# Kernel optimization log

Hardware: AMD Instinct MI355X
Metric: run time of the kernel (lower is better)

## Reference

```python
import jax, jax.numpy as jnp
import numpy as np
from jax import lax

GROUPS = 32
GN_EPS = 1e-3  # keras GroupNormalization default


def setup_inputs() -> dict:
    key = jax.random.key(0)
    ks = jax.random.split(key, 3)
    b, h, w, c = 16, 64, 64, 1024
    cg = c // GROUPS
    x = jax.random.normal(ks[0], (b, h, w, c), dtype=jnp.float32)
    w1 = jax.random.normal(ks[1], (cg, cg), dtype=jnp.float32) * (1.0 / np.sqrt(cg))
    b1 = jnp.zeros((cg,), jnp.float32)
    w3 = jax.random.normal(ks[2], (3, 3, cg, cg), dtype=jnp.float32) * (1.0 / np.sqrt(9 * cg))
    b3 = jnp.zeros((cg,), jnp.float32)
    gn_gamma = jnp.ones((cg,), jnp.float32)
    gn_beta = jnp.zeros((cg,), jnp.float32)
    return {"x": x, "w1": w1, "b1": b1, "w3": w3, "b3": b3,
            "gn_gamma": gn_gamma, "gn_beta": gn_beta}


def reference(x, w1, b1, w3, b3, gn_gamma, gn_beta):
    b, h, w, c = x.shape
    cg = c // GROUPS
    bg = b * GROUPS
    gx = x.reshape(bg, h, w, cg)

    # adaptive pools to 1 along one spatial axis
    x_h = jnp.mean(gx, axis=2, keepdims=True)                      # (bg, h, 1, cg)
    x_w = jnp.transpose(jnp.mean(gx, axis=1, keepdims=True), (0, 2, 1, 3))  # (bg, w, 1, cg)

    # 1x1 conv on concatenated strip (width==1) == matmul over channels
    hw = jnp.concatenate([x_h, x_w], axis=1)                       # (bg, h+w, 1, cg)
    hw = jnp.einsum('bsoc,cd->bsod', hw, w1) + b1
    x_h, x_w = hw[:, :h], hw[:, h:]
    x_w = jnp.transpose(x_w, (0, 2, 1, 3))                         # (bg, 1, w, cg)

    gated = gx * jax.nn.sigmoid(x_h) * jax.nn.sigmoid(x_w)

    # GroupNorm with groups == cg over cg channels -> per-channel norm over (h, w)
    mu = jnp.mean(gated, axis=(1, 2), keepdims=True)
    var = jnp.var(gated, axis=(1, 2), keepdims=True)
    x1 = (gated - mu) * lax.rsqrt(var + GN_EPS) * gn_gamma + gn_beta

    # 3x3 same conv
    x2 = lax.conv_general_dilated(gx, w3, (1, 1), 'SAME',
                                  dimension_numbers=('NHWC', 'HWIO', 'NHWC')) + b3

    # channel attention: softmax over global-avg-pooled channels
    x11 = jax.nn.softmax(jnp.mean(x1, axis=(1, 2)), axis=-1)       # (bg, cg)
    x21 = jax.nn.softmax(jnp.mean(x2, axis=(1, 2)), axis=-1)       # (bg, cg)
    # raw reshape (memory reinterpretation, matches TF code exactly)
    x12 = x2.reshape(bg, cg, h * w)
    x22 = x1.reshape(bg, cg, h * w)

    weights = (jnp.einsum('bc,bcl->bl', x11, x12) +
               jnp.einsum('bc,bcl->bl', x21, x22)).reshape(bg, h, w, 1)
    return (gx * jax.nn.sigmoid(weights)).reshape(b, h, w, c)
```

## Files before the change

### kernel.cpp

```cpp
#include <hip/hip_runtime.h>

typedef __bf16 bf16x8 __attribute__((ext_vector_type(8)));
typedef float floatx4 __attribute__((ext_vector_type(4)));

__device__ __forceinline__ float sigmoidf_(float v) {
    return 1.0f / (1.0f + __expf(-v));
}

extern "C" __global__ __launch_bounds__(512, 4)
void ema_fused(const float* __restrict__ x, const float* __restrict__ w1,
               const float* __restrict__ b1, const float* __restrict__ w3,
               const float* __restrict__ b3, const float* __restrict__ gamma,
               const float* __restrict__ beta, float* __restrict__ out)
{
    __shared__ float sm[17952];
    const int t = threadIdx.x;
    const int b = blockIdx.x;
    const float* gx = x + (size_t)b * 131072;
    float* gout = out + (size_t)b * 131072;

    const int c = t & 31;
    const int k = t >> 5;
    const int lane = t & 63;
    const int wave = t >> 6;
    const int nf = wave & 1;
    const int wbase = (wave >> 1) * 16;
    const int m_ = lane & 15;
    const int q_ = lane >> 4;

    float* rowsum = sm;
    float* colsum = sm + 2112;
    float* G      = sm;
    float* T1     = sm + 4096;
    float* astage = sm + 4224;
    float* shl    = sm + 8192;
    float* swl    = sm + 10240;
    __bf16* ringbase = (__bf16*)(sm + 12288);
    float*  sgbuf    = sm + 12288;
    __bf16* zrow     = (__bf16*)(sm + 16512);
    float* x21    = sm + 17568;
    float* x11    = sm + 17600;
    float* a1v    = sm + 17632;
    float* a0v    = sm + 17664;
    float* b3c    = sm + 17696;
    float* corners= sm + 17728;
    float* Stot   = sm + 17856;
    float* meanx2 = sm + 17888;

    float colacc[4];
#pragma unroll
    for (int i = 0; i < 4; ++i) colacc[i] = 0.f;

    for (int h8 = 0; h8 < 8; ++h8) {
#pragma unroll
        for (int j = 0; j < 8; ++j) {
            int h = h8 * 8 + j;
            float part = 0.f;
#pragma unroll
            for (int i = 0; i < 4; ++i) {
                int w = k + 16 * i;
                float v = gx[(h * 64 + w) * 32 + c];
                colacc[i] += v;
                part += v;
                if ((h == 0 || h == 63) && w == 0)
                    corners[((h == 63) ? 2 : 0) * 32 + c] = v;
                if ((h == 0 || h == 63) && w == 63)
                    corners[((h == 63) ? 3 : 1) * 32 + c] = v;
            }
            astage[(j * 16 + k) * 32 + c] = part;
        }
        __syncthreads();
        if (t < 256) {
            int j2 = t >> 5, c2 = t & 31;
            float s = 0.f;
#pragma unroll
            for (int k2 = 0; k2 < 16; ++k2) s += astage[(j2 * 16 + k2) * 32 + c2];
            rowsum[(h8 * 8 + j2) * 33 + c2] = s;
        }
        __syncthreads();
    }
#pragma unroll
    for (int i = 0; i < 4; ++i) colsum[(k + 16 * i) * 33 + c] = colacc[i];
    __syncthreads();

    {
        const int hh = t >> 3;
        const int d0 = (t & 7) * 4;
        float acch[4], accw[4];
#pragma unroll
        for (int kk = 0; kk < 4; ++kk) { acch[kk] = b1[d0 + kk]; accw[kk] = b1[d0 + kk]; }
        for (int ci = 0; ci < 32; ++ci) {
            float rs = rowsum[hh * 33 + ci] * (1.f / 64.f);
            float cs = colsum[hh * 33 + ci] * (1.f / 64.f);
#pragma unroll
            for (int kk = 0; kk < 4; ++kk) {
                float wv = w1[ci * 32 + d0 + kk];
                acch[kk] += rs * wv;
                accw[kk] += cs * wv;
            }
        }
#pragma unroll
        for (int kk = 0; kk < 4; ++kk) {
            shl[hh * 32 + d0 + kk] = sigmoidf_(acch[kk]);
            swl[hh * 32 + d0 + kk] = sigmoidf_(accw[kk]);
        }
    }
    if (t < 32) {
        float s = 0.f;
        for (int h = 0; h < 64; ++h) s += rowsum[h * 33 + t];
        Stot[t] = s;
        b3c[t] = b3[t];
    }
    __syncthreads();
    if (t < 32) {
        int co = t;
        float acc = 0.f;
        for (int dh = -1; dh <= 1; ++dh)
            for (int dw = -1; dw <= 1; ++dw) {
                int ks = (dh + 1) * 3 + (dw + 1);
                for (int ci = 0; ci < 32; ++ci) {
                    float S = Stot[ci];
                    if (dh == -1) S -= rowsum[63 * 33 + ci];
                    if (dh ==  1) S -= rowsum[ci];
                    if (dw == -1) S -= colsum[63 * 33 + ci];
                    if (dw ==  1) S -= colsum[ci];
                    if (dh == -1 && dw == -1) S += corners[3 * 32 + ci];
                    if (dh == -1 && dw ==  1) S += corners[2 * 32 + ci];
                    if (dh ==  1 && dw == -1) S += corners[1 * 32 + ci];
                    if (dh ==  1 && dw ==  1) S += corners[0 * 32 + ci];
                    acc += w3[ks * 1024 + ci * 32 + co] * S;
                }
            }
        meanx2[co] = acc * (1.f / 4096.f) + b3[co];
    }
    __syncthreads();
    if (t == 0) {
        float m = meanx2[0];
        for (int i = 1; i < 32; ++i) m = fmaxf(m, meanx2[i]);
        float s = 0.f;
        for (int i = 0; i < 32; ++i) { float e = __expf(meanx2[i] - m); x21[i] = e; s += e; }
        float inv = 1.f / s;
        for (int i = 0; i < 32; ++i) x21[i] *= inv;
    } else if (t == 64) {
        float m = -1e30f;
        for (int i = 0; i < 32; ++i) m = fmaxf(m, beta[i]);
        float s = 0.f;
        for (int i = 0; i < 32; ++i) s += __expf(beta[i] - m);
        float inv = 1.f / s;
        for (int i = 0; i < 32; ++i) x11[i] = __expf(beta[i] - m) * inv;
    }
    __syncthreads();

    bf16x8 Bf[9];
    {
        int ci0 = (lane >> 4) * 8;
        int co  = (lane & 15) + nf * 16;
#pragma unroll
        for (int ks = 0; ks < 9; ++ks) {
            bf16x8 v;
#pragma unroll
            for (int j = 0; j < 8; ++j)
                v[j] = (__bf16)w3[ks * 1024 + (ci0 + j) * 32 + co];
            Bf[ks] = v;
        }
    }

    for (int i = t; i < 4096; i += 512) G[i] = 0.f;
    for (int i = t; i < 1056; i += 512) sm[16512 + i] = 0.f;
    if (t < 256) {
        int s = t >> 6, colsel = (t >> 5) & 1, cc = t & 31;
        ringbase[s * 2112 + (colsel ? 65 * 32 : 0) + cc] = (__bf16)0.f;
    }
    __syncthreads();

    float sumg = 0.f, sumg2 = 0.f;
    float T1a0[4] = {0.f, 0.f, 0.f, 0.f};
    float T1a1[4] = {0.f, 0.f, 0.f, 0.f};
    float pre[4];

    auto issue = [&](int r) {
#pragma unroll
        for (int i = 0; i < 4; ++i)
            pre[i] = gx[(r * 64 + k + 16 * i) * 32 + c];
    };
    auto commit = [&](int r) {
        __bf16* rowp = ringbase + (r & 3) * 2112;
        float coef = x21[r >> 1];
        int par = (r & 1) << 11;
        float sr = shl[r * 32 + c];
#pragma unroll
        for (int i = 0; i < 4; ++i) {
            int w = k + 16 * i;
            float v = pre[i];
            rowp[(w + 1) * 32 + c] = (__bf16)v;
            float g = v * sr * swl[w * 32 + c];
            sumg += g; sumg2 += g * g;
            G[par + w * 32 + c] += coef * g;
        }
    };
    auto conv_row = [&](int h) -> floatx4 {
        floatx4 acc = {0.f, 0.f, 0.f, 0.f};
#pragma unroll
        for (int dh = -1; dh <= 1; ++dh) {
            int r = h + dh;
            const __bf16* rowp = (r < 0 || r > 63) ? zrow : (ringbase + (r & 3) * 2112);
#pragma unroll
            for (int dw = -1; dw <= 1; ++dw) {
                int ks = (dh + 1) * 3 + (dw + 1);
                const __bf16* ap = rowp + (wbase + m_ + dw + 1) * 32 + q_ * 8;
                bf16x8 av = *(const bf16x8*)ap;
                acc = __builtin_amdgcn_mfma_f32_16x16x32_bf16(av, Bf[ks], acc, 0, 0, 0);
            }
        }
        return acc;
    };

    issue(0); commit(0); issue(1);
    for (int h2 = 0; h2 < 32; ++h2) {
        {
            const int h = 2 * h2;
            commit(h + 1);
            if (h < 62) issue(h + 2);
            __syncthreads();
            floatx4 acc = conv_row(h);
            float coef = x11[h2];
#pragma unroll
            for (int rr = 0; rr < 4; ++rr) T1a0[rr] += coef * acc[rr];
        }
        {
            const int h = 2 * h2 + 1;
            if (h < 63) commit(h + 1);
            if (h < 62) issue(h + 2);
            __syncthreads();
            floatx4 acc = conv_row(h);
            float coef = x11[h2];
#pragma unroll
            for (int rr = 0; rr < 4; ++rr) T1a1[rr] += coef * acc[rr];
        }
    }

    {
        const int colw = m_ + nf * 16;
#pragma unroll
        for (int rr = 0; rr < 4; ++rr) {
            int w = wbase + q_ * 4 + rr;
            T1[w * 32 + colw]        = T1a0[rr];
            T1[2048 + w * 32 + colw] = T1a1[rr];
        }
    }
    shl[k * 32 + c] = sumg;
    shl[512 + k * 32 + c] = sumg2;
    __syncthreads();

    if (t < 32) {
        float S = 0.f, S2 = 0.f;
#pragma unroll
        for (int kk = 0; kk < 16; ++kk) { S += shl[kk * 32 + t]; S2 += shl[512 + kk * 32 + t]; }
        float mu  = S * (1.f / 4096.f);
        float var = S2 * (1.f / 4096.f) - mu * mu;
        float rs  = rsqrtf(var + 0.001f);
        float g1  = gamma[t] * rs;
        a1v[t] = g1;
        a0v[t] = beta[t] - g1 * mu;
    }
    __syncthreads();

#pragma unroll 2
    for (int idx = t; idx < 4096; idx += 512) {
        int cp = idx & 31;
        float wt = T1[idx] + b3c[cp] + a1v[cp] * G[idx] + a0v[cp];
        sgbuf[idx] = sigmoidf_(wt);
    }
    __syncthreads();

    {
        const floatx4* gx4 = (const floatx4*)gx;
        floatx4* gout4 = (floatx4*)gout;
#pragma unroll 4
        for (int j = 0; j < 64; ++j) {
            int idx4 = t + 512 * j;
            float s = sgbuf[idx4 >> 3];
            floatx4 v = gx4[idx4];
            v[0] *= s; v[1] *= s; v[2] *= s; v[3] *= s;
            gout4[idx4] = v;
        }
    }
}

extern "C" void kernel_launch(void* const* d_in, const int* in_sizes, int n_in,
                              void* d_out, int out_size, void* d_ws, size_t ws_size,
                              hipStream_t stream) {
    const float* x  = (const float*)d_in[0];
    const float* w1 = (const float*)d_in[1];
    const float* b1 = (const float*)d_in[2];
    const float* w3 = (const float*)d_in[3];
    const float* b3 = (const float*)d_in[4];
    const float* gg = (const float*)d_in[5];
    const float* gb = (const float*)d_in[6];
    float* out = (float*)d_out;
    hipLaunchKernelGGL(ema_fused, dim3(512), dim3(512), 0, stream,
                       x, w1, b1, w3, b3, gg, gb, out);
}
```

Baseline: 719.4 us.

## Vectorize row loads, deepen prefetch ring, and swizzle LDS conv buffers

Reworks the fused EMA kernel so each thread loads float4 vectors per row instead of scalar strided loads, and computes row sums with cross-lane shuffles instead of a larger shared staging buffer. The conv input ring grows from 4 to 6 slots with XOR-swizzled bf16 layout to reduce LDS bank conflicts, and rows are prefetched several steps ahead so two rows are committed and convolved per barrier, halving the synchronization count. Padded strides for G, shl and swl avoid bank conflicts. It costs more shared memory and more registers for prefetched rows, which may reduce occupancy.

```diff
diff --git a/kernel.cpp b/kernel.cpp
--- a/kernel.cpp
+++ b/kernel.cpp
@@ -1,6 +1,7 @@
 #include <hip/hip_runtime.h>
 
 typedef __bf16 bf16x8 __attribute__((ext_vector_type(8)));
+typedef __bf16 bf16x4 __attribute__((ext_vector_type(4)));
 typedef float floatx4 __attribute__((ext_vector_type(4)));
 
 __device__ __forceinline__ float sigmoidf_(float v) {
@@ -13,14 +14,15 @@
                const float* __restrict__ b3, const float* __restrict__ gamma,
                const float* __restrict__ beta, float* __restrict__ out)
 {
-    __shared__ float sm[17952];
+    __shared__ float sm[19616];
     const int t = threadIdx.x;
     const int b = blockIdx.x;
     const float* gx = x + (size_t)b * 131072;
     float* gout = out + (size_t)b * 131072;
-
-    const int c = t & 31;
-    const int k = t >> 5;
+    const floatx4* gx4 = (const floatx4*)gx;
+
+    const int wA = t >> 3;
+    const int c0 = (t & 7) * 4;
     const int lane = t & 63;
     const int wave = t >> 6;
     const int nf = wave & 1;
@@ -31,56 +33,64 @@
     float* rowsum = sm;
     float* colsum = sm + 2112;
     float* G      = sm;
-    float* T1     = sm + 4096;
-    float* astage = sm + 4224;
-    float* shl    = sm + 8192;
-    float* swl    = sm + 10240;
-    __bf16* ringbase = (__bf16*)(sm + 12288);
-    float*  sgbuf    = sm + 12288;
-    __bf16* zrow     = (__bf16*)(sm + 16512);
-    float* x21    = sm + 17568;
-    float* x11    = sm + 17600;
-    float* a1v    = sm + 17632;
-    float* a0v    = sm + 17664;
-    float* b3c    = sm + 17696;
-    float* corners= sm + 17728;
-    float* Stot   = sm + 17856;
-    float* meanx2 = sm + 17888;
-
-    float colacc[4];
-#pragma unroll
-    for (int i = 0; i < 4; ++i) colacc[i] = 0.f;
-
+    float* T1     = sm + 4608;
+    float* astage = sm + 4608;
+    float* shl    = sm + 8704;
+    float* swl    = sm + 10816;
+    __bf16* ringbase = (__bf16*)(sm + 12928);
+    float*  sgbuf    = sm + 12928;
+    float* x21    = sm + 19264;
+    float* x11    = sm + 19296;
+    float* a1v    = sm + 19328;
+    float* a0v    = sm + 19360;
+    float* b3c    = sm + 19392;
+    float* corners= sm + 19424;
+    float* Stot   = sm + 19552;
+    float* meanx2 = sm + 19584;
+
+    floatx4 colacc4 = {0.f, 0.f, 0.f, 0.f};
     for (int h8 = 0; h8 < 8; ++h8) {
+        floatx4 rv[8];
+#pragma unroll
+        for (int j = 0; j < 8; ++j) rv[j] = gx4[(h8 * 8 + j) * 512 + t];
+#pragma unroll
+        for (int j = 0; j < 8; ++j) colacc4 += rv[j];
+        if (h8 == 0 && (wA == 0 || wA == 63)) {
+            int ci = (wA == 63) ? 1 : 0;
+#pragma unroll
+            for (int i2 = 0; i2 < 4; ++i2) corners[ci * 32 + c0 + i2] = rv[0][i2];
+        }
+        if (h8 == 7 && (wA == 0 || wA == 63)) {
+            int ci = (wA == 63) ? 3 : 2;
+#pragma unroll
+            for (int i2 = 0; i2 < 4; ++i2) corners[ci * 32 + c0 + i2] = rv[7][i2];
+        }
 #pragma unroll
         for (int j = 0; j < 8; ++j) {
-            int h = h8 * 8 + j;
-            float part = 0.f;
-#pragma unroll
-            for (int i = 0; i < 4; ++i) {
-                int w = k + 16 * i;
-                float v = gx[(h * 64 + w) * 32 + c];
-                colacc[i] += v;
-                part += v;
-                if ((h == 0 || h == 63) && w == 0)
-                    corners[((h == 63) ? 2 : 0) * 32 + c] = v;
-                if ((h == 0 || h == 63) && w == 63)
-                    corners[((h == 63) ? 3 : 1) * 32 + c] = v;
+            floatx4 s = rv[j];
+#pragma unroll
+            for (int i2 = 0; i2 < 4; ++i2) {
+                float v = s[i2];
+                v += __shfl_xor(v, 8);
+                v += __shfl_xor(v, 16);
+                v += __shfl_xor(v, 32);
+                s[i2] = v;
             }
-            astage[(j * 16 + k) * 32 + c] = part;
+            if (lane < 8)
+                *(floatx4*)&astage[(j * 8 + wave) * 32 + lane * 4] = s;
         }
         __syncthreads();
         if (t < 256) {
             int j2 = t >> 5, c2 = t & 31;
             float s = 0.f;
 #pragma unroll
-            for (int k2 = 0; k2 < 16; ++k2) s += astage[(j2 * 16 + k2) * 32 + c2];
+            for (int wv = 0; wv < 8; ++wv) s += astage[(j2 * 8 + wv) * 32 + c2];
             rowsum[(h8 * 8 + j2) * 33 + c2] = s;
         }
         __syncthreads();
     }
 #pragma unroll
-    for (int i = 0; i < 4; ++i) colsum[(k + 16 * i) * 33 + c] = colacc[i];
+    for (int i = 0; i < 4; ++i) colsum[wA * 33 + c0 + i] = colacc4[i];
     __syncthreads();
 
     {
@@ -101,8 +111,8 @@
         }
 #pragma unroll
         for (int kk = 0; kk < 4; ++kk) {
-            shl[hh * 32 + d0 + kk] = sigmoidf_(acch[kk]);
-            swl[hh * 32 + d0 + kk] = sigmoidf_(accw[kk]);
+            shl[hh * 33 + d0 + kk] = sigmoidf_(acch[kk]);
+            swl[hh * 33 + d0 + kk] = sigmoidf_(accw[kk]);
         }
     }
     if (t < 32) {
@@ -151,10 +161,22 @@
     }
     __syncthreads();
 
+    floatx4 swv;
+#pragma unroll
+    for (int i = 0; i < 4; ++i) swv[i] = swl[wA * 33 + c0 + i];
+    const int swzW = (((wA + 1) >> 1) & 3) << 4;
+    const int wrOff = (wA + 1) * 64 + ((c0 * 2) ^ swzW);
+    int rdOff[3];
+#pragma unroll
+    for (int dwi = 0; dwi < 3; ++dwi) {
+        int W = wbase + m_ + dwi;
+        rdOff[dwi] = W * 64 + ((q_ * 16) ^ ((((W >> 1) & 3)) << 4));
+    }
+
     bf16x8 Bf[9];
     {
-        int ci0 = (lane >> 4) * 8;
-        int co  = (lane & 15) + nf * 16;
+        int ci0 = q_ * 8;
+        int co  = m_ + nf * 16;
 #pragma unroll
         for (int ks = 0; ks < 9; ++ks) {
             bf16x8 v;
@@ -165,78 +187,70 @@
         }
     }
 
-    for (int i = t; i < 4096; i += 512) G[i] = 0.f;
-    for (int i = t; i < 1056; i += 512) sm[16512 + i] = 0.f;
-    if (t < 256) {
-        int s = t >> 6, colsel = (t >> 5) & 1, cc = t & 31;
-        ringbase[s * 2112 + (colsel ? 65 * 32 : 0) + cc] = (__bf16)0.f;
-    }
-    __syncthreads();
-
-    float sumg = 0.f, sumg2 = 0.f;
-    float T1a0[4] = {0.f, 0.f, 0.f, 0.f};
-    float T1a1[4] = {0.f, 0.f, 0.f, 0.f};
-    float pre[4];
-
-    auto issue = [&](int r) {
+    for (int i = t; i < 4608; i += 512) G[i] = 0.f;
+    if (t < 192) {
+        int s = t >> 5, which = (t >> 4) & 1, i16 = t & 15;
+        ((float*)ringbase)[s * 1056 + (which ? 65 * 16 : 0) + i16] = 0.f;
+    }
+    __syncthreads();
+
+    floatx4 sumg4 = {0.f,0.f,0.f,0.f}, sumg24 = {0.f,0.f,0.f,0.f};
+    float T1a0[4] = {0.f,0.f,0.f,0.f};
+    float T1a1[4] = {0.f,0.f,0.f,0.f};
+
+    auto loadrow = [&](int r) -> floatx4 { return gx4[r * 512 + t]; };
+
+    auto commit = [&](int r, floatx4 v) {
+        int slot = r % 6;
+        float coef = x21[r >> 1];
+        floatx4 g;
 #pragma unroll
         for (int i = 0; i < 4; ++i)
-            pre[i] = gx[(r * 64 + k + 16 * i) * 32 + c];
+            g[i] = v[i] * shl[r * 33 + c0 + i] * swv[i];
+        sumg4 += g;
+        sumg24 += g * g;
+        bf16x4 pk;
+#pragma unroll
+        for (int i = 0; i < 4; ++i) pk[i] = (__bf16)v[i];
+        *(bf16x4*)((char*)ringbase + slot * 4224 + wrOff) = pk;
+        int par = (r & 1) * 2304;
+        floatx4* gp = (floatx4*)&G[par + wA * 36 + c0];
+        *gp += coef * g;
     };
-    auto commit = [&](int r) {
-        __bf16* rowp = ringbase + (r & 3) * 2112;
-        float coef = x21[r >> 1];
-        int par = (r & 1) << 11;
-        float sr = shl[r * 32 + c];
-#pragma unroll
-        for (int i = 0; i < 4; ++i) {
-            int w = k + 16 * i;
-            float v = pre[i];
-            rowp[(w + 1) * 32 + c] = (__bf16)v;
-            float g = v * sr * swl[w * 32 + c];
-            sumg += g; sumg2 += g * g;
-            G[par + w * 32 + c] += coef * g;
-        }
-    };
-    auto conv_row = [&](int h) -> floatx4 {
+
+    auto conv_row = [&](int h, float* T1a) {
         floatx4 acc = {0.f, 0.f, 0.f, 0.f};
 #pragma unroll
         for (int dh = -1; dh <= 1; ++dh) {
             int r = h + dh;
-            const __bf16* rowp = (r < 0 || r > 63) ? zrow : (ringbase + (r & 3) * 2112);
-#pragma unroll
-            for (int dw = -1; dw <= 1; ++dw) {
-                int ks = (dh + 1) * 3 + (dw + 1);
-                const __bf16* ap = rowp + (wbase + m_ + dw + 1) * 32 + q_ * 8;
-                bf16x8 av = *(const bf16x8*)ap;
-                acc = __builtin_amdgcn_mfma_f32_16x16x32_bf16(av, Bf[ks], acc, 0, 0, 0);
+            if (r < 0 || r > 63) continue;
+            const char* slotp = (const char*)ringbase + (r % 6) * 4224;
+#pragma unroll
+            for (int dwi = 0; dwi < 3; ++dwi) {
+                bf16x8 av = *(const bf16x8*)(slotp + rdOff[dwi]);
+                acc = __builtin_amdgcn_mfma_f32_16x16x32_bf16(av, Bf[(dh + 1) * 3 + dwi], acc, 0, 0, 0);
             }
         }
-        return acc;
+        float coef = x11[h >> 1];
+#pragma unroll
+        for (int rr = 0; rr < 4; ++rr) T1a[rr] += coef * acc[rr];
     };
 
-    issue(0); commit(0); issue(1);
-    for (int h2 = 0; h2 < 32; ++h2) {
-        {
-            const int h = 2 * h2;
-            commit(h + 1);
-            if (h < 62) issue(h + 2);
-            __syncthreads();
-            floatx4 acc = conv_row(h);
-            float coef = x11[h2];
-#pragma unroll
-            for (int rr = 0; rr < 4; ++rr) T1a0[rr] += coef * acc[rr];
-        }
-        {
-            const int h = 2 * h2 + 1;
-            if (h < 63) commit(h + 1);
-            if (h < 62) issue(h + 2);
-            __syncthreads();
-            floatx4 acc = conv_row(h);
-            float coef = x11[h2];
-#pragma unroll
-            for (int rr = 0; rr < 4; ++rr) T1a1[rr] += coef * acc[rr];
-        }
+    floatx4 pB0, pB1, pA0, pA1;
+    pB0 = loadrow(0);
+    commit(0, pB0);
+    pB0 = loadrow(1); pB1 = loadrow(2);
+    pA0 = loadrow(3); pA1 = loadrow(4);
+
+    for (int h = 0; h < 64; h += 2) {
+        commit(h + 1, pB0);
+        if (h + 2 < 64) commit(h + 2, pB1);
+        pB0 = pA0; pB1 = pA1;
+        if (h + 5 < 64) pA0 = loadrow(h + 5);
+        if (h + 6 < 64) pA1 = loadrow(h + 6);
+        __syncthreads();
+        conv_row(h, T1a0);
+        conv_row(h + 1, T1a1);
     }
 
     {
@@ -248,14 +262,16 @@
             T1[2048 + w * 32 + colw] = T1a1[rr];
         }
     }
-    shl[k * 32 + c] = sumg;
-    shl[512 + k * 32 + c] = sumg2;
+#pragma unroll
+    for (int i = 0; i < 4; ++i) {
+        shl[wA * 33 + c0 + i] = sumg4[i];
+        swl[wA * 33 + c0 + i] = sumg24[i];
+    }
     __syncthreads();
 
     if (t < 32) {
         float S = 0.f, S2 = 0.f;
-#pragma unroll
-        for (int kk = 0; kk < 16; ++kk) { S += shl[kk * 32 + t]; S2 += shl[512 + kk * 32 + t]; }
+        for (int w2 = 0; w2 < 64; ++w2) { S += shl[w2 * 33 + t]; S2 += swl[w2 * 33 + t]; }
         float mu  = S * (1.f / 4096.f);
         float var = S2 * (1.f / 4096.f) - mu * mu;
         float rs  = rsqrtf(var + 0.001f);
@@ -268,13 +284,14 @@
 #pragma unroll 2
     for (int idx = t; idx < 4096; idx += 512) {
         int cp = idx & 31;
-        float wt = T1[idx] + b3c[cp] + a1v[cp] * G[idx] + a0v[cp];
+        int wv2 = (idx >> 5) & 63;
+        int par = (idx >> 11) * 2304;
+        float wt = T1[idx] + b3c[cp] + a1v[cp] * G[par + wv2 * 36 + cp] + a0v[cp];
         sgbuf[idx] = sigmoidf_(wt);
     }
     __syncthreads();
 
     {
-        const floatx4* gx4 = (const floatx4*)gx;
         floatx4* gout4 = (floatx4*)gout;
 #pragma unroll 4
         for (int j = 0; j < 64; ++j) {
```

Measured after the change: 606.8 us. 15.6% less time.
